# Optimization experiments

Hardware: AMD Instinct MI355X
Metric: run time of the kernel (lower is better)

Reference implementation:

```python
import jax, jax.numpy as jnp
import numpy as np

N_HEADS = 16

def setup_inputs() -> dict:
    key = jax.random.key(0)
    ks = jax.random.split(key, 5)
    C = 1024
    B, T = 2, 2048
    s_in = 1.0 / np.sqrt(C)
    x = jax.random.normal(ks[0], (B, T, C), dtype=jnp.float32)
    W_qkv = jax.random.normal(ks[1], (C, 3 * C), dtype=jnp.float32) * s_in
    b_qkv = jnp.zeros((3 * C,), dtype=jnp.float32)
    W_proj = jax.random.normal(ks[2], (C, C), dtype=jnp.float32) * s_in
    b_proj = jnp.zeros((C,), dtype=jnp.float32)
    return {"x": x, "W_qkv": W_qkv, "b_qkv": b_qkv, "W_proj": W_proj, "b_proj": b_proj}

def reference(x, W_qkv, b_qkv, W_proj, b_proj):
    B, T, C = x.shape
    H = N_HEADS
    D = C // H  # head dim
    qkv = x @ W_qkv + b_qkv                      # [B,T,3C]
    q, k, v = jnp.split(qkv, 3, axis=-1)
    # [B,T,C] -> [B,H,T,D]
    q = q.reshape(B, T, H, D).transpose(0, 2, 1, 3)
    k = k.reshape(B, T, H, D).transpose(0, 2, 1, 3)
    v = v.reshape(B, T, H, D).transpose(0, 2, 1, 3)
    scale = 1.0 / np.sqrt(D)
    att = jnp.einsum('bhqd,bhkd->bhqk', q, k) * scale  # [B,H,T,T]
    causal = jnp.tril(jnp.ones((T, T), dtype=bool))
    att = jnp.where(causal[None, None], att, -jnp.inf)
    att = jax.nn.softmax(att, axis=-1)
    y = jnp.einsum('bhqk,bhkd->bhqd', att, v)    # [B,H,T,D]
    y = y.transpose(0, 2, 1, 3).reshape(B, T, C)
    return y @ W_proj + b_proj
```

## Files before the change

### kernel.cpp

```cpp
#include <hip/hip_runtime.h>
#include <hip/hip_bf16.h>
#include <stdint.h>

#define DEVI __device__ __forceinline__

typedef __attribute__((ext_vector_type(8))) short bf16x8;
typedef __attribute__((ext_vector_type(4))) float f32x4;
typedef __attribute__((ext_vector_type(4))) short short4v;
typedef __attribute__((ext_vector_type(4))) float float4v;
typedef __attribute__((ext_vector_type(2))) unsigned int uint2v;

#define QSCALE 0.1803368801111204f

DEVI unsigned short f2bf(float f) {
  union { float f; unsigned u; } v; v.f = f;
  unsigned r = v.u + 0x7FFFu + ((v.u >> 16) & 1u);
  return (unsigned short)(r >> 16);
}

DEVI unsigned cvt_pk_bf16(float lo, float hi) {
  unsigned r;
  asm("v_cvt_pk_bf16_f32 %0, %1, %2" : "=v"(r) : "v"(lo), "v"(hi));
  return r;
}

DEVI void async16(unsigned short* lds, const unsigned short* g) {
  __builtin_amdgcn_global_load_lds(
      (const __attribute__((address_space(1))) void*)g,
      (__attribute__((address_space(3))) void*)lds, 16, 0, 0);
}

DEVI int xcd_swz_flat() {
  int orig = (int)blockIdx.x + (int)gridDim.x * (int)blockIdx.y;
  int cpx = ((int)gridDim.x * (int)gridDim.y) >> 3;
  return (orig & 7) * cpx + (orig >> 3);
}

__global__ void k_f32_to_bf16(const float* __restrict__ in,
                              unsigned short* __restrict__ out, int n4) {
  int i = blockIdx.x * 256 + threadIdx.x;
  if (i < n4) {
    float4v f = *reinterpret_cast<const float4v*>(in + (size_t)i * 4);
    short4v o;
#pragma unroll
    for (int j = 0; j < 4; ++j) o[j] = (short)f2bf(f[j]);
    *reinterpret_cast<short4v*>(out + (size_t)i * 4) = o;
  }
}

__global__ void k_wt(const float* __restrict__ W, unsigned short* __restrict__ Wt,
                     int K, int N) {
  __shared__ float tile[32][33];
  int n0 = blockIdx.x * 32, k0 = blockIdx.y * 32;
  int r = threadIdx.x >> 5, c = threadIdx.x & 31;
#pragma unroll
  for (int i = 0; i < 4; ++i)
    tile[r + i * 8][c] = W[(size_t)(k0 + r + i * 8) * N + n0 + c];
  __syncthreads();
#pragma unroll
  for (int i = 0; i < 4; ++i)
    Wt[(size_t)(n0 + r + i * 8) * K + k0 + c] = f2bf(tile[c][r + i * 8]);
}

DEVI void stage_ab(unsigned short* AsB, unsigned short* BsB,
                   const unsigned short* Ab, const unsigned short* Bb,
                   int K, int k0, int tid) {
#pragma unroll
  for (int it = 0; it < 2; ++it) {
    int c = it * 256 + tid;
    int row = c >> 2, cc = (c & 3) * 8;
    async16(&AsB[c * 8], Ab + (size_t)row * K + k0 + cc);
    async16(&BsB[c * 8], Bb + (size_t)row * K + k0 + cc);
  }
}

template <int EPI>
__global__ void k_gemm(const unsigned short* __restrict__ A,
                       const unsigned short* __restrict__ Bt,
                       const float* __restrict__ bias,
                       void* __restrict__ outp, int M, int N, int K) {
  __shared__ __align__(16) unsigned short As[2][128 * 32];
  __shared__ __align__(16) unsigned short Bs[2][128 * 32];
  const int tid = threadIdx.x;
  const int swzf = xcd_swz_flat();
  const int m0 = (swzf / (int)gridDim.x) * 128, n0 = (swzf % (int)gridDim.x) * 128;
  const int lane = tid & 63, w = tid >> 6;
  const int wr = (w >> 1) * 64, wc = (w & 1) * 64;
  const int lr = lane & 15, lg = lane >> 4;
  f32x4 acc[4][4] = {};
  const unsigned short* Ab = A + (size_t)m0 * K;
  const unsigned short* Bb = Bt + (size_t)n0 * K;

  const int ns = K >> 5;
  stage_ab(As[0], Bs[0], Ab, Bb, K, 0, tid);
  stage_ab(As[1], Bs[1], Ab, Bb, K, 32, tid);
  asm volatile("s_waitcnt vmcnt(4)" ::: "memory");
  __builtin_amdgcn_s_barrier();
  __builtin_amdgcn_sched_barrier(0);

  for (int s = 0; s < ns; ++s) {
    const int cur = s & 1;
    bf16x8 af[4], bfr[4];
#pragma unroll
    for (int m = 0; m < 4; ++m)
      af[m] = *reinterpret_cast<const bf16x8*>(&As[cur][(wr + m * 16 + lr) * 32 + lg * 8]);
#pragma unroll
    for (int n = 0; n < 4; ++n)
      bfr[n] = *reinterpret_cast<const bf16x8*>(&Bs[cur][(wc + n * 16 + lr) * 32 + lg * 8]);
#pragma unroll
    for (int m = 0; m < 4; ++m)
#pragma unroll
      for (int n = 0; n < 4; ++n)
        acc[m][n] = __builtin_amdgcn_mfma_f32_16x16x32_bf16(af[m], bfr[n], acc[m][n], 0, 0, 0);
    __builtin_amdgcn_s_barrier();
    const int ks = (s + 2 < ns) ? (s + 2) * 32 : 0;
    stage_ab(As[cur], Bs[cur], Ab, Bb, K, ks, tid);
    asm volatile("s_waitcnt vmcnt(4)" ::: "memory");
    __builtin_amdgcn_s_barrier();
    __builtin_amdgcn_sched_barrier(0);
  }
  if (EPI == 0) {
    unsigned short* qkv = (unsigned short*)outp;
#pragma unroll
    for (int n = 0; n < 4; ++n) {
      int col = n0 + wc + n * 16 + lr;
      float bv = bias[col];
      int sel = col >> 10, cc = col & 1023;
      int h = cc >> 6, d = cc & 63;
      float sc = (sel == 0) ? QSCALE : 1.0f;
#pragma unroll
      for (int m = 0; m < 4; ++m) {
#pragma unroll
        for (int r = 0; r < 4; ++r) {
          int row = m0 + wr + m * 16 + lg * 4 + r;
          int bh = ((row >> 11) << 4) + h;
          int t = row & 2047;
          qkv[((size_t)(sel * 32 + bh) * 2048 + t) * 64 + d] = f2bf((acc[m][n][r] + bv) * sc);
        }
      }
    }
  } else {
    float* O = (float*)outp;
#pragma unroll
    for (int n = 0; n < 4; ++n) {
      int col = n0 + wc + n * 16 + lr;
      float bv = bias[col];
#pragma unroll
      for (int m = 0; m < 4; ++m)
#pragma unroll
        for (int r = 0; r < 4; ++r) {
          int row = m0 + wr + m * 16 + lg * 4 + r;
          O[(size_t)row * N + col] = acc[m][n][r] + bv;
        }
    }
  }
}

__global__ __launch_bounds__(256)
void k_gemmP(const unsigned short* __restrict__ A,
             const unsigned short* __restrict__ Bt,
             const float* __restrict__ bias,
             float* __restrict__ O, int M, int N, int K) {
  __shared__ __align__(16) unsigned short As[2][128 * 32];
  __shared__ __align__(16) unsigned short Bs[2][64 * 32];
  const int tid = threadIdx.x;
  const int swzf = xcd_swz_flat();
  const int m0 = (swzf / (int)gridDim.x) * 128, n0 = (swzf % (int)gridDim.x) * 64;
  const int lane = tid & 63, w = tid >> 6;
  const int wr = (w >> 1) * 64, wc = (w & 1) * 32;
  const int lr = lane & 15, lg = lane >> 4;
  f32x4 acc[4][2] = {};
  const unsigned short* Ab = A + (size_t)m0 * K;
  const unsigned short* Bb = Bt + (size_t)n0 * K;

  auto stage = [&](unsigned short* AsB, unsigned short* BsB, int k0) {
#pragma unroll
    for (int it = 0; it < 2; ++it) {
      int c = it * 256 + tid;
      int row = c >> 2, cc = (c & 3) * 8;
      async16(&AsB[c * 8], Ab + (size_t)row * K + k0 + cc);
    }
    int row = tid >> 2, cc = (tid & 3) * 8;
    async16(&BsB[tid * 8], Bb + (size_t)row * K + k0 + cc);
  };

  const int ns = K >> 5;
  stage(As[0], Bs[0], 0);
  stage(As[1], Bs[1], 32);
  asm volatile("s_waitcnt vmcnt(3)" ::: "memory");
  __builtin_amdgcn_s_barrier();
  __builtin_amdgcn_sched_barrier(0);

  for (int s = 0; s < ns; ++s) {
    const int cur = s & 1;
    bf16x8 af[4], bfr[2];
#pragma unroll
    for (int m = 0; m < 4; ++m)
      af[m] = *reinterpret_cast<const bf16x8*>(&As[cur][(wr + m * 16 + lr) * 32 + lg * 8]);
#pragma unroll
    for (int n = 0; n < 2; ++n)
      bfr[n] = *reinterpret_cast<const bf16x8*>(&Bs[cur][(wc + n * 16 + lr) * 32 + lg * 8]);
#pragma unroll
    for (int m = 0; m < 4; ++m)
#pragma unroll
      for (int n = 0; n < 2; ++n)
        acc[m][n] = __builtin_amdgcn_mfma_f32_16x16x32_bf16(af[m], bfr[n], acc[m][n], 0, 0, 0);
    __builtin_amdgcn_s_barrier();
    const int ks = (s + 2 < ns) ? (s + 2) * 32 : 0;
    stage(As[cur], Bs[cur], ks);
    asm volatile("s_waitcnt vmcnt(3)" ::: "memory");
    __builtin_amdgcn_s_barrier();
    __builtin_amdgcn_sched_barrier(0);
  }
#pragma unroll
  for (int n = 0; n < 2; ++n) {
    int col = n0 + wc + n * 16 + lr;
    float bv = bias[col];
#pragma unroll
    for (int m = 0; m < 4; ++m)
#pragma unroll
      for (int r = 0; r < 4; ++r) {
        int row = m0 + wr + m * 16 + lg * 4 + r;
        O[(size_t)row * N + col] = acc[m][n][r] + bv;
      }
  }
}

__global__ void k_vt(const unsigned short* __restrict__ V,
                     unsigned short* __restrict__ Vt) {
  __shared__ __align__(16) unsigned short t[64][72];
  int bh = blockIdx.y, t0 = blockIdx.x * 64;
  int r = threadIdx.x >> 3, c8 = (threadIdx.x & 7) * 8;
#pragma unroll
  for (int i = 0; i < 2; ++i) {
    int row = i * 32 + r;
    *reinterpret_cast<bf16x8*>(&t[row][c8]) =
        *reinterpret_cast<const bf16x8*>(&V[((size_t)bh * 2048 + t0 + row) * 64 + c8]);
  }
  __syncthreads();
#pragma unroll
  for (int i = 0; i < 2; ++i) {
    int d = i * 32 + r;
    bf16x8 o;
#pragma unroll
    for (int j = 0; j < 8; ++j) o[j] = (short)t[c8 + j][d];
    *reinterpret_cast<bf16x8*>(&Vt[((size_t)bh * 64 + d) * 2048 + t0 + c8]) = o;
  }
}

DEVI void stage_kv(unsigned short* KsB, unsigned short* VsB,
                   const unsigned short* Kbh, const unsigned short* Vbh,
                   int k0, int tid, int srow, int gcol) {
  async16(&KsB[tid * 8], Kbh + (size_t)(k0 + srow) * 64 + gcol);
  async16(&VsB[tid * 8], Vbh + (size_t)srow * 2048 + k0 + gcol);
}

DEVI void attn_store(unsigned short* __restrict__ Y, int bh, int qw, int lg, int lr,
                     const f32x4* o, float l_run) {
  const int b = bh >> 4, h = bh & 15;
  float rl = 1.0f / l_run;
  float rlo[4];
#pragma unroll
  for (int r = 0; r < 4; ++r) rlo[r] = __shfl(rl, lg * 4 + r, 64);
#pragma unroll
  for (int r = 0; r < 4; ++r) {
    int t = qw + lg * 4 + r;
#pragma unroll
    for (int n = 0; n < 4; ++n)
      Y[((size_t)(b * 2048 + t)) * 1024 + h * 64 + n * 16 + lr] = f2bf(o[n][r] * rlo[r]);
  }
}

__global__ __launch_bounds__(512)
void k_attn(const unsigned short* __restrict__ Qg,
            const unsigned short* __restrict__ Kg,
            const unsigned short* __restrict__ Vtg,
            unsigned short* __restrict__ Y) {
  __shared__ __align__(16) unsigned short Ks[2][64 * 64];
  __shared__ __align__(16) unsigned short Vs[2][64 * 64];
  __shared__ __align__(16) unsigned short Ps[8][16 * 64];
  const int swzf = xcd_swz_flat();
  const int bh = swzf >> 3;
  const int x = swzf & 7;
  const int xa = 15 - x;
  const int xb = x;
  const int n0 = 2 * xa + 2;
  const int nt = 34;
  const int tid = threadIdx.x, lane = tid & 63, w = tid >> 6;
  const int lr = lane & 15, lg = lane >> 4;
  const int swz = (lane & 7) * 8;
  const int psw = (lr & 7) * 8;
  const unsigned short* Kbh = Kg + (size_t)bh * 2048 * 64;
  const unsigned short* Vbh = Vtg + (size_t)bh * 64 * 2048;

  const int qwA = xa * 128 + w * 16, qwB = xb * 128 + w * 16;
  const unsigned short* QrA = Qg + ((size_t)bh * 2048 + qwA + lr) * 64;
  const unsigned short* QrB = Qg + ((size_t)bh * 2048 + qwB + lr) * 64;
  bf16x8 qa0A = *reinterpret_cast<const bf16x8*>(&QrA[lg * 8]);
  bf16x8 qa1A = *reinterpret_cast<const bf16x8*>(&QrA[32 + lg * 8]);
  bf16x8 qa0B = *reinterpret_cast<const bf16x8*>(&QrB[lg * 8]);
  bf16x8 qa1B = *reinterpret_cast<const bf16x8*>(&QrB[32 + lg * 8]);

  float m_run = -1e30f, l_run = 0.f;
  f32x4 o[4] = {};
  int qw = qwA;
  bf16x8 qa0 = qa0A, qa1 = qa1A;

  const int srow = tid >> 3;
  const int gcol = ((tid & 7) ^ (srow & 7)) * 8;

  stage_kv(Ks[0], Vs[0], Kbh, Vbh, 0, tid, srow, gcol);
  stage_kv(Ks[1], Vs[1], Kbh, Vbh, 64, tid, srow, gcol);
  asm volatile("s_waitcnt vmcnt(2)" ::: "memory");
  __builtin_amdgcn_s_barrier();
  __builtin_amdgcn_sched_barrier(0);

  for (int t = 0; t < nt; ++t) {
    if (t == n0) {
      attn_store(Y, bh, qwA, lg, lr, o, l_run);
      m_run = -1e30f; l_run = 0.f;
#pragma unroll
      for (int n = 0; n < 4; ++n) o[n] = (f32x4){0.f, 0.f, 0.f, 0.f};
      qw = qwB; qa0 = qa0B; qa1 = qa1B;
    }
    const int cur = t & 1;
    const int k0 = ((t < n0) ? t : (t - n0)) * 64;
    if (k0 <= qw + 15) {
      const unsigned short* KsC = Ks[cur];
      const unsigned short* VsC = Vs[cur];

      f32x4 s[4];
      __builtin_amdgcn_s_setprio(1);
#pragma unroll
      for (int n = 0; n < 4; ++n) {
        bf16x8 kb0 = *reinterpret_cast<const bf16x8*>(&KsC[(n * 16 + lr) * 64 + ((lg * 8) ^ swz)]);
        bf16x8 kb1 = *reinterpret_cast<const bf16x8*>(&KsC[(n * 16 + lr) * 64 + ((32 + lg * 8) ^ swz)]);
        f32x4 z = {0.f, 0.f, 0.f, 0.f};
        z = __builtin_amdgcn_mfma_f32_16x16x32_bf16(kb0, qa0, z, 0, 0, 0);
        z = __builtin_amdgcn_mfma_f32_16x16x32_bf16(kb1, qa1, z, 0, 0, 0);
        s[n] = z;
      }
      __builtin_amdgcn_s_setprio(0);
      if (k0 + 63 > qw) {
        const int klim = qw + lr - k0 - lg * 4;
#pragma unroll
        for (int n = 0; n < 4; ++n)
#pragma unroll
          for (int r = 0; r < 4; ++r)
            if (n * 16 + r > klim) s[n][r] = -1e30f;
      }
      float tmax = s[0][0];
#pragma unroll
      for (int n = 0; n < 4; ++n)
#pragma unroll
        for (int r = 0; r < 4; ++r) tmax = fmaxf(tmax, s[n][r]);
      tmax = fmaxf(tmax, __shfl_xor(tmax, 16, 64));
      tmax = fmaxf(tmax, __shfl_xor(tmax, 32, 64));
      if (__any(tmax > m_run + 11.5f)) {
        float mNew = fmaxf(m_run, tmax);
        float alpha = __builtin_exp2f(m_run - mNew);
        m_run = mNew;
        l_run *= alpha;
        float ao[4];
#pragma unroll
        for (int r = 0; r < 4; ++r) ao[r] = __shfl(alpha, lg * 4 + r, 64);
#pragma unroll
        for (int n = 0; n < 4; ++n)
#pragma unroll
          for (int r = 0; r < 4; ++r) o[n][r] *= ao[r];
      }
      float tsum = 0.f;
#pragma unroll
      for (int n = 0; n < 4; ++n)
#pragma unroll
        for (int r = 0; r < 4; ++r) {
          s[n][r] = __builtin_exp2f(s[n][r] - m_run);
          tsum += s[n][r];
        }
      tsum += __shfl_xor(tsum, 16, 64);
      tsum += __shfl_xor(tsum, 32, 64);
      l_run += tsum;
#pragma unroll
      for (int n = 0; n < 4; ++n) {
        uint2v pk;
        pk[0] = cvt_pk_bf16(s[n][0], s[n][1]);
        pk[1] = cvt_pk_bf16(s[n][2], s[n][3]);
        *reinterpret_cast<uint2v*>(&Ps[w][lr * 64 + ((n * 16 + lg * 4) ^ psw)]) = pk;
      }
      __builtin_amdgcn_s_setprio(1);
#pragma unroll
      for (int jj = 0; jj < 2; ++jj) {
        bf16x8 pa = *reinterpret_cast<const bf16x8*>(&Ps[w][lr * 64 + ((jj * 32 + lg * 8) ^ psw)]);
#pragma unroll
        for (int n = 0; n < 4; ++n) {
          bf16x8 vb = *reinterpret_cast<const bf16x8*>(
              &VsC[(n * 16 + lr) * 64 + ((jj * 32 + lg * 8) ^ swz)]);
          o[n] = __builtin_amdgcn_mfma_f32_16x16x32_bf16(pa, vb, o[n], 0, 0, 0);
        }
      }
      __builtin_amdgcn_s_setprio(0);
    }
    __builtin_amdgcn_s_barrier();
    {
      const int ts = (t + 2 < nt) ? (t + 2) : 0;
      const int kS = ((ts < n0) ? ts : (ts - n0)) * 64;
      stage_kv(Ks[cur], Vs[cur], Kbh, Vbh, kS, tid, srow, gcol);
    }
    asm volatile("s_waitcnt vmcnt(2)" ::: "memory");
    __builtin_amdgcn_s_barrier();
    __builtin_amdgcn_sched_barrier(0);
  }
  attn_store(Y, bh, qwB, lg, lr, o, l_run);
}

extern "C" void kernel_launch(void* const* d_in, const int* in_sizes, int n_in,
                              void* d_out, int out_size, void* d_ws, size_t ws_size,
                              hipStream_t stream) {
  const float* x     = (const float*)d_in[0];
  const float* Wqkv  = (const float*)d_in[1];
  const float* bqkv  = (const float*)d_in[2];
  const float* Wproj = (const float*)d_in[3];
  const float* bproj = (const float*)d_in[4];
  float* out = (float*)d_out;

  uint8_t* ws = (uint8_t*)d_ws;
  unsigned short* xb     = (unsigned short*)(ws);
  unsigned short* wqkvT  = (unsigned short*)(ws + ((size_t)8  << 20));
  unsigned short* wprojT = (unsigned short*)(ws + ((size_t)14 << 20));
  unsigned short* qkvb   = (unsigned short*)(ws + ((size_t)16 << 20));
  unsigned short* vt     = (unsigned short*)(ws + ((size_t)40 << 20));

  k_f32_to_bf16<<<4096, 256, 0, stream>>>(x, xb, 1048576);
  k_wt<<<dim3(96, 32), 256, 0, stream>>>(Wqkv, wqkvT, 1024, 3072);
  k_wt<<<dim3(32, 32), 256, 0, stream>>>(Wproj, wprojT, 1024, 1024);
  k_gemm<0><<<dim3(24, 32), 256, 0, stream>>>(xb, wqkvT, bqkv, qkvb, 4096, 3072, 1024);
  k_vt<<<dim3(32, 32), 256, 0, stream>>>(qkvb + (size_t)2 * 32 * 2048 * 64, vt);
  k_attn<<<dim3(8, 32), 512, 0, stream>>>(qkvb, qkvb + (size_t)32 * 2048 * 64, vt, xb);
  k_gemmP<<<dim3(16, 32), 256, 0, stream>>>(xb, wprojT, bproj, out, 4096, 1024, 1024);
}
```

Baseline: 127.0 us.

## Triple-buffer K/V tiles and software-pipeline QK^T one tile ahead

Grows the shared-memory K/V ring from two to three buffers and prefetches three tiles ahead. The QK^T MFMA for the next tile is issued before the softmax and PV of the current tile, so matrix work overlaps with the exp/reduction VALU work. The cost is more LDS use, which may lower occupancy, and extra live score registers. The vmcnt wait count is left unchanged, which may not match the deeper pipeline.

After: 130.0 us. +2.4%, slower.

```diff
diff --git a/kernel.cpp b/kernel.cpp
--- a/kernel.cpp
+++ b/kernel.cpp
@@ -271,19 +271,31 @@
   }
 }
 
+DEVI void qk_compute(f32x4* s, const unsigned short* KsC,
+                     bf16x8 qa0, bf16x8 qa1, int lr, int lg, int swz) {
+#pragma unroll
+  for (int n = 0; n < 4; ++n) {
+    bf16x8 kb0 = *reinterpret_cast<const bf16x8*>(&KsC[(n * 16 + lr) * 64 + ((lg * 8) ^ swz)]);
+    bf16x8 kb1 = *reinterpret_cast<const bf16x8*>(&KsC[(n * 16 + lr) * 64 + ((32 + lg * 8) ^ swz)]);
+    f32x4 z = {0.f, 0.f, 0.f, 0.f};
+    z = __builtin_amdgcn_mfma_f32_16x16x32_bf16(kb0, qa0, z, 0, 0, 0);
+    z = __builtin_amdgcn_mfma_f32_16x16x32_bf16(kb1, qa1, z, 0, 0, 0);
+    s[n] = z;
+  }
+}
+
 __global__ __launch_bounds__(512)
 void k_attn(const unsigned short* __restrict__ Qg,
             const unsigned short* __restrict__ Kg,
             const unsigned short* __restrict__ Vtg,
             unsigned short* __restrict__ Y) {
-  __shared__ __align__(16) unsigned short Ks[2][64 * 64];
-  __shared__ __align__(16) unsigned short Vs[2][64 * 64];
+  __shared__ __align__(16) unsigned short Ks[3][64 * 64];
+  __shared__ __align__(16) unsigned short Vs[3][64 * 64];
   __shared__ __align__(16) unsigned short Ps[8][16 * 64];
   const int swzf = xcd_swz_flat();
   const int bh = swzf >> 3;
   const int x = swzf & 7;
   const int xa = 15 - x;
-  const int xb = x;
   const int n0 = 2 * xa + 2;
   const int nt = 34;
   const int tid = threadIdx.x, lane = tid & 63, w = tid >> 6;
@@ -293,7 +305,7 @@
   const unsigned short* Kbh = Kg + (size_t)bh * 2048 * 64;
   const unsigned short* Vbh = Vtg + (size_t)bh * 64 * 2048;
 
-  const int qwA = xa * 128 + w * 16, qwB = xb * 128 + w * 16;
+  const int qwA = xa * 128 + w * 16, qwB = x * 128 + w * 16;
   const unsigned short* QrA = Qg + ((size_t)bh * 2048 + qwA + lr) * 64;
   const unsigned short* QrB = Qg + ((size_t)bh * 2048 + qwB + lr) * 64;
   bf16x8 qa0A = *reinterpret_cast<const bf16x8*>(&QrA[lg * 8]);
@@ -304,56 +316,59 @@
   float m_run = -1e30f, l_run = 0.f;
   f32x4 o[4] = {};
   int qw = qwA;
-  bf16x8 qa0 = qa0A, qa1 = qa1A;
 
   const int srow = tid >> 3;
   const int gcol = ((tid & 7) ^ (srow & 7)) * 8;
 
   stage_kv(Ks[0], Vs[0], Kbh, Vbh, 0, tid, srow, gcol);
   stage_kv(Ks[1], Vs[1], Kbh, Vbh, 64, tid, srow, gcol);
+  stage_kv(Ks[2], Vs[2], Kbh, Vbh, 128, tid, srow, gcol);
   asm volatile("s_waitcnt vmcnt(2)" ::: "memory");
   __builtin_amdgcn_s_barrier();
   __builtin_amdgcn_sched_barrier(0);
 
+  f32x4 sN[4];
+  qk_compute(sN, Ks[0], qa0A, qa1A, lr, lg, swz);
+
   for (int t = 0; t < nt; ++t) {
+    const int cur = t % 3;
+    f32x4 sC[4];
+#pragma unroll
+    for (int n = 0; n < 4; ++n) sC[n] = sN[n];
+    if (t + 1 < nt) {
+      const bool nB = (t + 1 >= n0);
+      const int k0n = (nB ? (t + 1 - n0) : (t + 1)) * 64;
+      const int qwn = nB ? qwB : qwA;
+      if (k0n <= qwn + 15) {
+        __builtin_amdgcn_s_setprio(1);
+        qk_compute(sN, Ks[(t + 1) % 3], nB ? qa0B : qa0A, nB ? qa1B : qa1A,
+                   lr, lg, swz);
+        __builtin_amdgcn_s_setprio(0);
+      }
+    }
     if (t == n0) {
       attn_store(Y, bh, qwA, lg, lr, o, l_run);
       m_run = -1e30f; l_run = 0.f;
 #pragma unroll
       for (int n = 0; n < 4; ++n) o[n] = (f32x4){0.f, 0.f, 0.f, 0.f};
-      qw = qwB; qa0 = qa0B; qa1 = qa1B;
-    }
-    const int cur = t & 1;
+      qw = qwB;
+    }
     const int k0 = ((t < n0) ? t : (t - n0)) * 64;
     if (k0 <= qw + 15) {
-      const unsigned short* KsC = Ks[cur];
       const unsigned short* VsC = Vs[cur];
-
-      f32x4 s[4];
-      __builtin_amdgcn_s_setprio(1);
-#pragma unroll
-      for (int n = 0; n < 4; ++n) {
-        bf16x8 kb0 = *reinterpret_cast<const bf16x8*>(&KsC[(n * 16 + lr) * 64 + ((lg * 8) ^ swz)]);
-        bf16x8 kb1 = *reinterpret_cast<const bf16x8*>(&KsC[(n * 16 + lr) * 64 + ((32 + lg * 8) ^ swz)]);
-        f32x4 z = {0.f, 0.f, 0.f, 0.f};
-        z = __builtin_amdgcn_mfma_f32_16x16x32_bf16(kb0, qa0, z, 0, 0, 0);
-        z = __builtin_amdgcn_mfma_f32_16x16x32_bf16(kb1, qa1, z, 0, 0, 0);
-        s[n] = z;
-      }
-      __builtin_amdgcn_s_setprio(0);
       if (k0 + 63 > qw) {
         const int klim = qw + lr - k0 - lg * 4;
 #pragma unroll
         for (int n = 0; n < 4; ++n)
 #pragma unroll
           for (int r = 0; r < 4; ++r)
-            if (n * 16 + r > klim) s[n][r] = -1e30f;
-      }
-      float tmax = s[0][0];
+            if (n * 16 + r > klim) sC[n][r] = -1e30f;
+      }
+      float tmax = sC[0][0];
 #pragma unroll
       for (int n = 0; n < 4; ++n)
 #pragma unroll
-        for (int r = 0; r < 4; ++r) tmax = fmaxf(tmax, s[n][r]);
+        for (int r = 0; r < 4; ++r) tmax = fmaxf(tmax, sC[n][r]);
       tmax = fmaxf(tmax, __shfl_xor(tmax, 16, 64));
       tmax = fmaxf(tmax, __shfl_xor(tmax, 32, 64));
       if (__any(tmax > m_run + 11.5f)) {
@@ -374,8 +389,8 @@
       for (int n = 0; n < 4; ++n)
 #pragma unroll
         for (int r = 0; r < 4; ++r) {
-          s[n][r] = __builtin_exp2f(s[n][r] - m_run);
-          tsum += s[n][r];
+          sC[n][r] = __builtin_exp2f(sC[n][r] - m_run);
+          tsum += sC[n][r];
         }
       tsum += __shfl_xor(tsum, 16, 64);
       tsum += __shfl_xor(tsum, 32, 64);
@@ -383,8 +398,8 @@
 #pragma unroll
       for (int n = 0; n < 4; ++n) {
         uint2v pk;
-        pk[0] = cvt_pk_bf16(s[n][0], s[n][1]);
-        pk[1] = cvt_pk_bf16(s[n][2], s[n][3]);
+        pk[0] = cvt_pk_bf16(sC[n][0], sC[n][1]);
+        pk[1] = cvt_pk_bf16(sC[n][2], sC[n][3]);
         *reinterpret_cast<uint2v*>(&Ps[w][lr * 64 + ((n * 16 + lg * 4) ^ psw)]) = pk;
       }
       __builtin_amdgcn_s_setprio(1);
@@ -402,7 +417,7 @@
     }
     __builtin_amdgcn_s_barrier();
     {
-      const int ts = (t + 2 < nt) ? (t + 2) : 0;
+      const int ts = (t + 3 < nt) ? (t + 3) : 0;
       const int kS = ((ts < n0) ? ts : (ts - n0)) * 64;
       stage_kv(Ks[cur], Vs[cur], Kbh, Vbh, kS, tid, srow, gcol);
     }
```

## Split paired causal query tiles into separate attention blocks

Applied to the files above, without the earlier changes.

Each attention block previously handled two complementary 128-row query tiles (a long one and a short one) in a single loop of 34 key tiles, balancing causal work per block. The change launches 512 blocks instead of 256, each handling one query tile. Blocks with the heavy tiles come first and the light tiles fill in afterwards. This doubles the parallelism and removes the mid-loop store/reset, but it relies on the hardware scheduler for load balancing and stages the first two KV tiles redundantly in more blocks.

Result: faster. 123.3 us (-2.9%).

```diff
diff --git a/kernel.cpp b/kernel.cpp
--- a/kernel.cpp
+++ b/kernel.cpp
@@ -279,13 +279,14 @@
   __shared__ __align__(16) unsigned short Ks[2][64 * 64];
   __shared__ __align__(16) unsigned short Vs[2][64 * 64];
   __shared__ __align__(16) unsigned short Ps[8][16 * 64];
-  const int swzf = xcd_swz_flat();
-  const int bh = swzf >> 3;
-  const int x = swzf & 7;
-  const int xa = 15 - x;
-  const int xb = x;
-  const int n0 = 2 * xa + 2;
-  const int nt = 34;
+  const int orig = (int)blockIdx.x;
+  const int slot = orig >> 8;
+  const int within = orig & 255;
+  const int sw = (within & 7) * 32 + (within >> 3);
+  const int bh = sw >> 3;
+  const int xp = sw & 7;
+  const int x = slot ? xp : (15 - xp);
+  const int nkt = 2 * x + 2;
   const int tid = threadIdx.x, lane = tid & 63, w = tid >> 6;
   const int lr = lane & 15, lg = lane >> 4;
   const int swz = (lane & 7) * 8;
@@ -293,18 +294,13 @@
   const unsigned short* Kbh = Kg + (size_t)bh * 2048 * 64;
   const unsigned short* Vbh = Vtg + (size_t)bh * 64 * 2048;
 
-  const int qwA = xa * 128 + w * 16, qwB = xb * 128 + w * 16;
-  const unsigned short* QrA = Qg + ((size_t)bh * 2048 + qwA + lr) * 64;
-  const unsigned short* QrB = Qg + ((size_t)bh * 2048 + qwB + lr) * 64;
-  bf16x8 qa0A = *reinterpret_cast<const bf16x8*>(&QrA[lg * 8]);
-  bf16x8 qa1A = *reinterpret_cast<const bf16x8*>(&QrA[32 + lg * 8]);
-  bf16x8 qa0B = *reinterpret_cast<const bf16x8*>(&QrB[lg * 8]);
-  bf16x8 qa1B = *reinterpret_cast<const bf16x8*>(&QrB[32 + lg * 8]);
+  const int qw = x * 128 + w * 16;
+  const unsigned short* Qrow = Qg + ((size_t)bh * 2048 + qw + lr) * 64;
+  bf16x8 qa0 = *reinterpret_cast<const bf16x8*>(&Qrow[lg * 8]);
+  bf16x8 qa1 = *reinterpret_cast<const bf16x8*>(&Qrow[32 + lg * 8]);
 
   float m_run = -1e30f, l_run = 0.f;
   f32x4 o[4] = {};
-  int qw = qwA;
-  bf16x8 qa0 = qa0A, qa1 = qa1A;
 
   const int srow = tid >> 3;
   const int gcol = ((tid & 7) ^ (srow & 7)) * 8;
@@ -315,16 +311,9 @@
   __builtin_amdgcn_s_barrier();
   __builtin_amdgcn_sched_barrier(0);
 
-  for (int t = 0; t < nt; ++t) {
-    if (t == n0) {
-      attn_store(Y, bh, qwA, lg, lr, o, l_run);
-      m_run = -1e30f; l_run = 0.f;
-#pragma unroll
-      for (int n = 0; n < 4; ++n) o[n] = (f32x4){0.f, 0.f, 0.f, 0.f};
-      qw = qwB; qa0 = qa0B; qa1 = qa1B;
-    }
+  for (int t = 0; t < nkt; ++t) {
     const int cur = t & 1;
-    const int k0 = ((t < n0) ? t : (t - n0)) * 64;
+    const int k0 = t * 64;
     if (k0 <= qw + 15) {
       const unsigned short* KsC = Ks[cur];
       const unsigned short* VsC = Vs[cur];
@@ -402,15 +391,14 @@
     }
     __builtin_amdgcn_s_barrier();
     {
-      const int ts = (t + 2 < nt) ? (t + 2) : 0;
-      const int kS = ((ts < n0) ? ts : (ts - n0)) * 64;
-      stage_kv(Ks[cur], Vs[cur], Kbh, Vbh, kS, tid, srow, gcol);
+      const int ts = (t + 2 < nkt) ? (t + 2) : 0;
+      stage_kv(Ks[cur], Vs[cur], Kbh, Vbh, ts * 64, tid, srow, gcol);
     }
     asm volatile("s_waitcnt vmcnt(2)" ::: "memory");
     __builtin_amdgcn_s_barrier();
     __builtin_amdgcn_sched_barrier(0);
   }
-  attn_store(Y, bh, qwB, lg, lr, o, l_run);
+  attn_store(Y, bh, qw, lg, lr, o, l_run);
 }
 
 extern "C" void kernel_launch(void* const* d_in, const int* in_sizes, int n_in,
@@ -435,6 +423,6 @@
   k_wt<<<dim3(32, 32), 256, 0, stream>>>(Wproj, wprojT, 1024, 1024);
   k_gemm<0><<<dim3(24, 32), 256, 0, stream>>>(xb, wqkvT, bqkv, qkvb, 4096, 3072, 1024);
   k_vt<<<dim3(32, 32), 256, 0, stream>>>(qkvb + (size_t)2 * 32 * 2048 * 64, vt);
-  k_attn<<<dim3(8, 32), 512, 0, stream>>>(qkvb, qkvb + (size_t)32 * 2048 * 64, vt, xb);
+  k_attn<<<dim3(512, 1), 512, 0, stream>>>(qkvb, qkvb + (size_t)32 * 2048 * 64, vt, xb);
   k_gemmP<<<dim3(16, 32), 256, 0, stream>>>(xb, wprojT, bproj, out, 4096, 1024, 1024);
 }
```
